# Kernel tuning notes

Hardware: AMD Instinct MI355X
Metric: run time of the kernel (lower is better)

The kernel has to match this reference:

```python
import jax, jax.numpy as jnp
import numpy as np

NN_SIZE = 10          # k for kNN (includes the point itself as its own nearest neighbor)
COS_EPS = 1e-8        # torch.nn.CosineSimilarity eps


def _pairwise_sqdist(p):
    # p: (B,N,3) -> (B,N,N) squared euclidean distances without (B,N,N,3) intermediate
    x2 = jnp.sum(p * p, axis=-1)                      # (B,N)
    inner = jnp.einsum('bnd,bmd->bnm', p, p)          # (B,N,N)
    return x2[:, :, None] + x2[:, None, :] - 2.0 * inner


def _batch_normals(points):
    # points: (B,N,3) -> PCA normals (B,N,3)
    d = _pairwise_sqdist(points)                      # (B,N,N)
    _, idx = jax.lax.top_k(-d, NN_SIZE)               # (B,N,K) indices of k nearest
    nbrs = jax.vmap(lambda p, i: p[i])(points, idx)   # (B,N,K,3) gathered neighborhoods
    centered = nbrs - jnp.mean(nbrs, axis=2, keepdims=True)
    cov = jnp.einsum('bnki,bnkj->bnij', centered, centered) / NN_SIZE  # (B,N,3,3)
    _, vecs = jnp.linalg.eigh(cov)                    # eigenvalues ascending
    return vecs[..., :, 0]                            # eigvec of smallest eigval = normal


def setup_inputs() -> dict:
    key = jax.random.key(0)
    k1, k2 = jax.random.split(key)
    pred = jax.random.normal(k1, (8, 4096, 3), dtype=jnp.float32)
    gt_normals = jax.random.normal(k2, (8, 4096, 3), dtype=jnp.float32)
    return {"pred": pred, "gt_normals": gt_normals}


def reference(pred, gt_normals):
    pred_normals = _batch_normals(pred)                         # (B,N,3)
    dot = jnp.sum(pred_normals * gt_normals, axis=-1)           # (B,N)
    na = jnp.linalg.norm(pred_normals, axis=-1)
    nb = jnp.linalg.norm(gt_normals, axis=-1)
    cos = dot / (jnp.maximum(na, COS_EPS) * jnp.maximum(nb, COS_EPS))
    return jnp.mean(1.0 - cos)
```

## Files before the change

### kernel.cpp

```cpp
#include <hip/hip_runtime.h>
#include <math.h>


#define NPTS   4096
#define KNN    10
#define NBINS  256
#define XLO    (-5.5f)
#define INVBW  (256.0f / 11.0f)
#define W      1536
#define QPB    32
#define NB     1024
#define LISTCAP 32768

__device__ __forceinline__ unsigned int umed3(unsigned int a, unsigned int b, unsigned int c) {
    unsigned int r;
    asm("v_med3_u32 %0, %1, %2, %3" : "=v"(r) : "v"(a), "v"(b), "v"(c));
    return r;
}

__device__ __forceinline__ void sift(unsigned int nd[KNN], unsigned int key) {
#pragma unroll
    for (int t = KNN - 1; t >= 1; --t)
        nd[t] = umed3(key, nd[t - 1], nd[t]);
    nd[0] = nd[0] < key ? nd[0] : key;
}

__device__ __forceinline__ int xbin(float x) {
    int bin = (int)floorf((x - XLO) * INVBW);
    return bin < 0 ? 0 : (bin > NBINS - 1 ? NBINS - 1 : bin);
}

#define MAKE_KEY(q, c, J)                                                     \
    ({                                                                        \
        float sw_ = (q).w + (c).w;                                            \
        float dp_ = fmaf((q).x, (c).x, fmaf((q).y, (c).y, (q).z * (c).z));    \
        float d_  = fmaf(-2.0f, dp_, sw_);                                    \
        d_ = fmaxf(d_, 0.0f);                                                 \
        (__float_as_uint(d_) & 0xFFFFF000u) | (unsigned)(J);                  \
    })

__device__ float normal_loss3f(const float nbx[KNN], const float nby[KNN],
                               const float nbz[KNN], const float* g3)
{
    float sx = 0.f, sy = 0.f, sz = 0.f;
#pragma unroll
    for (int t = 0; t < KNN; ++t) { sx += nbx[t]; sy += nby[t]; sz += nbz[t]; }
    float mx = sx * 0.1f, my = sy * 0.1f, mz = sz * 0.1f;
    float c00 = 0.f, c01 = 0.f, c02 = 0.f, c11 = 0.f, c12 = 0.f, c22 = 0.f;
#pragma unroll
    for (int t = 0; t < KNN; ++t) {
        float ux = nbx[t] - mx, uy = nby[t] - my, uz = nbz[t] - mz;
        c00 = fmaf(ux, ux, c00);
        c01 = fmaf(ux, uy, c01);
        c02 = fmaf(ux, uz, c02);
        c11 = fmaf(uy, uy, c11);
        c12 = fmaf(uy, uz, c12);
        c22 = fmaf(uz, uz, c22);
    }
    float a00 = c00 * 0.1f, a01 = c01 * 0.1f, a02 = c02 * 0.1f;
    float a11 = c11 * 0.1f, a12 = c12 * 0.1f, a22 = c22 * 0.1f;

    float vx = 1.0f, vy = 0.0f, vz = 0.0f;
    float qd = (a00 + a11 + a22) * (1.0f / 3.0f);
    float p1 = a01 * a01 + a02 * a02 + a12 * a12;
    float b00 = a00 - qd, b11 = a11 - qd, b22 = a22 - qd;
    float p2 = b00 * b00 + b11 * b11 + b22 * b22 + 2.0f * p1;
    if (p2 > 1e-30f) {
        float p   = sqrtf(p2 * (1.0f / 6.0f));
        float inv = 1.0f / p;
        float m00 = b00 * inv, m01 = a01 * inv, m02 = a02 * inv;
        float m11 = b11 * inv, m12 = a12 * inv, m22 = b22 * inv;
        float detB = m00 * (m11 * m22 - m12 * m12)
                   - m01 * (m01 * m22 - m12 * m02)
                   + m02 * (m01 * m12 - m11 * m02);
        float r = 0.5f * detB;
        r = r < -1.0f ? -1.0f : (r > 1.0f ? 1.0f : r);
        float phi  = acosf(r) * (1.0f / 3.0f);
        float eig0 = qd + 2.0f * p * cosf(phi + 2.0943951023931953f);
        float r0x = a00 - eig0, r0y = a01, r0z = a02;
        float r1y = a11 - eig0, r1z = a12;
        float r2z = a22 - eig0;
        float c0x = r0y * r1z - r0z * r1y;
        float c0y = r0z * r0y - r0x * r1z;
        float c0z = r0x * r1y - r0y * r0y;
        float c1x = r0y * r2z - r0z * r1z;
        float c1y = r0z * r0z - r0x * r2z;
        float c1z = r0x * r1z - r0y * r0z;
        float c2x = r1y * r2z - r1z * r1z;
        float c2y = r1z * r0z - r0y * r2z;
        float c2z = r0y * r1z - r1y * r0z;
        float n0 = c0x * c0x + c0y * c0y + c0z * c0z;
        float n1 = c1x * c1x + c1y * c1y + c1z * c1z;
        float n2 = c2x * c2x + c2y * c2y + c2z * c2z;
        float bx, by, bz, bn;
        if (n0 >= n1 && n0 >= n2) { bx = c0x; by = c0y; bz = c0z; bn = n0; }
        else if (n1 >= n2)        { bx = c1x; by = c1y; bz = c1z; bn = n1; }
        else                      { bx = c2x; by = c2y; bz = c2z; bn = n2; }
        if (bn > 1e-30f) {
            float s = rsqrtf(bn);
            vx = bx * s; vy = by * s; vz = bz * s;
        }
    }
    float gx = g3[0], gy = g3[1], gz = g3[2];
    float dotg = vx * gx + vy * gy + vz * gz;
    float na = sqrtf(vx * vx + vy * vy + vz * vz);
    float gn = sqrtf(gx * gx + gy * gy + gz * gz);
    float cs = dotg / (fmaxf(na, 1e-8f) * fmaxf(gn, 1e-8f));
    return 1.0f - cs;
}

__global__ __launch_bounds__(1024) void gtnl_bin(
    const float* __restrict__ pred, float4* __restrict__ wsPts,
    unsigned int* __restrict__ wsCnt)
{
    __shared__ unsigned int hist[NBINS];
    __shared__ unsigned int bst[NBINS + 1];

    const int tid = threadIdx.x;
    const int b   = blockIdx.x;
    if (b == 0 && tid == 0) wsCnt[0] = 0;
    const float* src = pred + (size_t)b * NPTS * 3;

    if (tid < NBINS) hist[tid] = 0;
    __syncthreads();

    float px[4], py[4], pz[4];
    int   pb[4], pidx[4];
#pragma unroll
    for (int k = 0; k < 4; ++k) {
        int p = tid + 1024 * k;
        float x = src[3 * p + 0];
        float y = src[3 * p + 1];
        float z = src[3 * p + 2];
        int bin = xbin(x);
        px[k] = x; py[k] = y; pz[k] = z; pb[k] = bin; pidx[k] = p;
        atomicAdd(&hist[bin], 1u);
    }
    __syncthreads();

    if (tid < 64) {
        unsigned s0 = hist[4 * tid + 0], s1 = hist[4 * tid + 1];
        unsigned s2 = hist[4 * tid + 2], s3 = hist[4 * tid + 3];
        unsigned tot = s0 + s1 + s2 + s3;
        unsigned pre = tot;
#pragma unroll
        for (int d = 1; d < 64; d <<= 1) {
            unsigned t = __shfl_up(pre, d, 64);
            if (tid >= d) pre += t;
        }
        unsigned ex = pre - tot;
        bst[4 * tid + 0] = ex;
        bst[4 * tid + 1] = ex + s0;
        bst[4 * tid + 2] = ex + s0 + s1;
        bst[4 * tid + 3] = ex + s0 + s1 + s2;
        if (tid == 63) bst[NBINS] = ex + tot;
    }
    __syncthreads();

    if (tid < NBINS) hist[tid] = bst[tid];
    __syncthreads();

#pragma unroll
    for (int k = 0; k < 4; ++k) {
        unsigned pos = atomicAdd(&hist[pb[k]], 1u);
        wsPts[(size_t)b * NPTS + pos] =
            make_float4(px[k], py[k], pz[k], __uint_as_float((unsigned)pidx[k]));
    }
}

__global__ __launch_bounds__(256, 8) void gtnl_scan(
    const float4* __restrict__ wsPts, const float* __restrict__ gt,
    float* __restrict__ qloss, unsigned int* __restrict__ wsCnt,
    unsigned int* __restrict__ wsList)
{
    __shared__ float4 pts[W];

    const int tid   = threadIdx.x;
    const int bid   = blockIdx.x;
    const int b     = bid >> 7;
    const int chunk = bid & 127;
    const int qbase = chunk * QPB;
    const int s     = tid & 7;
    const int ql    = tid >> 3;

    int W0 = qbase + QPB / 2 - W / 2;
    W0 = W0 < 0 ? 0 : (W0 > NPTS - W ? NPTS - W : W0);

    const float4* wp = wsPts + (size_t)b * NPTS;
    for (int i = tid; i < W; i += 256) {
        float4 v = wp[W0 + i];
        pts[i] = make_float4(v.x, v.y, v.z, fmaf(v.x, v.x, fmaf(v.y, v.y, v.z * v.z)));
    }
    __syncthreads();

    const int qpos = qbase + ql;
    const float4 q = pts[qpos - W0];

    unsigned int nd[KNN];
#pragma unroll
    for (int t = 0; t < KNN; ++t) nd[t] = 0x7F000000u;

#pragma unroll 2
    for (int t = 0; t < W / 8; ++t) {
        int j = 8 * t + s;
        float4 c = pts[j];
        sift(nd, MAKE_KEY(q, c, j));
    }

#pragma unroll
    for (int r = 1; r <= 4; r <<= 1) {
        unsigned int tmp[KNN];
#pragma unroll
        for (int t = 0; t < KNN; ++t) tmp[t] = nd[t];
#pragma unroll
        for (int t = 0; t < KNN; ++t) {
            unsigned int pk = (unsigned int)__shfl_xor((int)tmp[t], r, 64);
            sift(nd, pk);
        }
    }

    unsigned int thr_bits = (nd[KNN - 1] & 0xFFFFF000u) + 0x1000u;
    float thr = __uint_as_float(thr_bits);
    float hw  = __uint_as_float(__float_as_uint(sqrtf(thr)) + 4) + 1e-3f;
    bool okL = (W0 == 0)        || (q.x - hw > pts[0].x);
    bool okR = (W0 == NPTS - W) || (q.x + hw < pts[W - 1].x);

    const unsigned int qorig = __float_as_uint(wp[qpos].w);
    if (okL && okR) {
        float nbx[KNN], nby[KNN], nbz[KNN];
#pragma unroll
        for (int t = 0; t < KNN; ++t) {
            float4 pn = pts[nd[t] & 0xFFFu];
            nbx[t] = pn.x; nby[t] = pn.y; nbz[t] = pn.z;
        }
        float res = normal_loss3f(nbx, nby, nbz, gt + ((size_t)b * NPTS + qorig) * 3);
        if (s == 0) qloss[(size_t)b * NPTS + qorig] = res;
    } else {
        if (s == 0) {
            unsigned int idx = atomicAdd(wsCnt, 1u);
            wsList[idx] = ((unsigned)b << 12) | (unsigned)qpos;
            qloss[(size_t)b * NPTS + qorig] = 0.0f;
        }
    }
}

__global__ __launch_bounds__(256, 4) void gtnl_fix(
    const float4* __restrict__ wsPts, const float* __restrict__ gt,
    float* __restrict__ qloss, const unsigned int* __restrict__ wsCnt,
    const unsigned int* __restrict__ wsList)
{
    const int lane = threadIdx.x & 63;
    const int wid  = blockIdx.x * 4 + (threadIdx.x >> 6);
    unsigned int n = wsCnt[0];

    for (unsigned int i = wid; i < n; i += 4096) {
        unsigned int e = wsList[i];
        const int b    = e >> 12;
        const int qpos = e & 0xFFF;
        const float4* wp = wsPts + (size_t)b * NPTS;

        float4 qv = wp[qpos];
        float4 q  = make_float4(qv.x, qv.y, qv.z,
                                fmaf(qv.x, qv.x, fmaf(qv.y, qv.y, qv.z * qv.z)));
        const unsigned int qorig = __float_as_uint(qv.w);

        unsigned int nd[KNN];
#pragma unroll
        for (int t = 0; t < KNN; ++t) nd[t] = 0x7F000000u;

#pragma unroll 8
        for (int t = 0; t < NPTS / 64; ++t) {
            int j = 64 * t + lane;
            float4 v = wp[j];
            float4 c = make_float4(v.x, v.y, v.z,
                                   fmaf(v.x, v.x, fmaf(v.y, v.y, v.z * v.z)));
            sift(nd, MAKE_KEY(q, c, j));
        }

        unsigned int keys[KNN];
#pragma unroll
        for (int r = 0; r < KNN; ++r) {
            unsigned int m = nd[0];
#pragma unroll
            for (int d = 1; d < 64; d <<= 1) {
                unsigned int o = __shfl_xor(m, d, 64);
                m = m < o ? m : o;
            }
            keys[r] = m;
            bool win = (nd[0] == m);
#pragma unroll
            for (int t = 0; t < KNN - 1; ++t) nd[t] = win ? nd[t + 1] : nd[t];
            nd[KNN - 1] = win ? 0xFFFFFFFFu : nd[KNN - 1];
        }

        float nbx[KNN], nby[KNN], nbz[KNN];
#pragma unroll
        for (int t = 0; t < KNN; ++t) {
            float4 pn = wp[keys[t] & 0xFFFu];
            nbx[t] = pn.x; nby[t] = pn.y; nbz[t] = pn.z;
        }
        float res = normal_loss3f(nbx, nby, nbz, gt + ((size_t)b * NPTS + qorig) * 3);
        if (lane == 0) qloss[(size_t)b * NPTS + qorig] = res;
    }
}

__global__ __launch_bounds__(1024) void gtnl_reduceQ(
    const float* __restrict__ qloss, float* __restrict__ out)
{
    __shared__ float sbuf[1024];
    const int tid = threadIdx.x;
    const float4* q4 = (const float4*)qloss;
    float s = 0.0f;
#pragma unroll
    for (int t = 0; t < 8; ++t) {
        float4 v = q4[tid + 1024 * t];
        s += (v.x + v.y) + (v.z + v.w);
    }
    sbuf[tid] = s;
    __syncthreads();
    for (int k = 512; k > 0; k >>= 1) {
        if (tid < k) sbuf[tid] += sbuf[tid + k];
        __syncthreads();
    }
    if (tid == 0) out[0] = sbuf[0] / 32768.0f;
}

__global__ __launch_bounds__(256) void gtnl_brute(
    const float* __restrict__ pred, const float* __restrict__ gt,
    float* __restrict__ partial)
{
    __shared__ float4 ptsB[NPTS];
    __shared__ unsigned int mbuf[64][3][KNN];

    const int tid = threadIdx.x;
    const int b   = blockIdx.x >> 6;
    const int qc  = blockIdx.x & 63;
    const int ql  = tid & 63;
    const int sub = tid >> 6;
    const int qi  = qc * 64 + ql;

    const float* src = pred + (size_t)b * NPTS * 3;
    for (int p = tid; p < NPTS; p += 256) {
        float x = src[3 * p + 0], y = src[3 * p + 1], z = src[3 * p + 2];
        ptsB[p] = make_float4(x, y, z, fmaf(x, x, fmaf(y, y, z * z)));
    }
    __syncthreads();

    const float4 q = ptsB[qi];
    unsigned int nd[KNN];
#pragma unroll
    for (int t = 0; t < KNN; ++t) nd[t] = 0xFFFFFFFFu;

    const int j0 = sub * 1024;
#pragma unroll 8
    for (int j = j0; j < j0 + 1024; ++j) {
        float4 c = ptsB[j];
        sift(nd, MAKE_KEY(q, c, j));
    }

    if (sub != 0) {
#pragma unroll
        for (int t = 0; t < KNN; ++t) mbuf[ql][sub - 1][t] = nd[t];
    }
    __syncthreads();

    float res = 0.0f;
    if (sub == 0) {
#pragma unroll
        for (int ss = 0; ss < 3; ++ss)
#pragma unroll
            for (int t = 0; t < KNN; ++t) sift(nd, mbuf[ql][ss][t]);
        float nbx[KNN], nby[KNN], nbz[KNN];
#pragma unroll
        for (int t = 0; t < KNN; ++t) {
            float4 pn = ptsB[nd[t] & 0xFFFu];
            nbx[t] = pn.x; nby[t] = pn.y; nbz[t] = pn.z;
        }
        res = normal_loss3f(nbx, nby, nbz, gt + ((size_t)b * NPTS + qi) * 3);
#pragma unroll
        for (int d = 32; d > 0; d >>= 1) res += __shfl_xor(res, d, 64);
    }
    __syncthreads();
    if (tid == 0) partial[blockIdx.x] = res;
}

__global__ __launch_bounds__(512) void gtnl_reduceP(
    const float* __restrict__ partial, float* __restrict__ out)
{
    __shared__ float sb[512];
    const int tid = threadIdx.x;
    sb[tid] = partial[tid];
    __syncthreads();
    for (int k = 256; k > 0; k >>= 1) {
        if (tid < k) sb[tid] += sb[tid + k];
        __syncthreads();
    }
    if (tid == 0) out[0] = sb[0] / 32768.0f;
}

extern "C" void kernel_launch(void* const* d_in, const int* in_sizes, int n_in,
                              void* d_out, int out_size, void* d_ws, size_t ws_size,
                              hipStream_t stream) {
    const float* pred = (const float*)d_in[0];
    const float* gt   = (const float*)d_in[1];
    float* out        = (float*)d_out;

    const size_t PTS_BYTES   = (size_t)8 * NPTS * sizeof(float4);
    const size_t QLOSS_BYTES = (size_t)8 * NPTS * sizeof(float);
    const size_t LIST_BYTES  = (size_t)LISTCAP * sizeof(unsigned);
    const size_t NEED = PTS_BYTES + QLOSS_BYTES + LIST_BYTES + 64;

    if (ws_size >= NEED) {
        float4*       wsPts  = (float4*)d_ws;
        float*        qloss  = (float*)((char*)d_ws + PTS_BYTES);
        unsigned int* wsList = (unsigned int*)((char*)d_ws + PTS_BYTES + QLOSS_BYTES);
        unsigned int* wsCnt  = (unsigned int*)((char*)d_ws + PTS_BYTES + QLOSS_BYTES + LIST_BYTES);

        gtnl_bin<<<8, 1024, 0, stream>>>(pred, wsPts, wsCnt);
        gtnl_scan<<<NB, 256, 0, stream>>>(wsPts, gt, qloss, wsCnt, wsList);
        gtnl_fix<<<NB, 256, 0, stream>>>(wsPts, gt, qloss, wsCnt, wsList);
        gtnl_reduceQ<<<1, 1024, 0, stream>>>(qloss, out);
    } else {
        float* partial = (float*)d_ws;
        gtnl_brute<<<512, 256, 0, stream>>>(pred, gt, partial);
        gtnl_reduceP<<<1, 512, 0, stream>>>(partial, out);
    }
}
```

Before: 54.19 us.

## Scan kNN window outward from center with early termination on x-distance bound

Reorders the shared-memory window so candidates are stored in alternating order outward from the query chunk center, enlarges the window, and adds a wave-wide early exit once both sides exceed the current kth-neighbor distance in x. Candidate insertions are also skipped when no lane would improve its top-k list. This aims to cut the number of distance evaluations and sifts per query and reduce fallback cases, at the cost of larger shared memory (lower occupancy via launch bounds 4) and extra divergence and ballot checks.

```diff
diff --git a/kernel.cpp b/kernel.cpp
--- a/kernel.cpp
+++ b/kernel.cpp
@@ -7,7 +7,7 @@
 #define NBINS  256
 #define XLO    (-5.5f)
 #define INVBW  (256.0f / 11.0f)
-#define W      1536
+#define W      2048
 #define QPB    32
 #define NB     1024
 #define LISTCAP 32768
@@ -168,7 +168,7 @@
     }
 }
 
-__global__ __launch_bounds__(256, 8) void gtnl_scan(
+__global__ __launch_bounds__(256, 4) void gtnl_scan(
     const float4* __restrict__ wsPts, const float* __restrict__ gt,
     float* __restrict__ qloss, unsigned int* __restrict__ wsCnt,
     unsigned int* __restrict__ wsList)
@@ -187,24 +187,49 @@
     W0 = W0 < 0 ? 0 : (W0 > NPTS - W ? NPTS - W : W0);
 
     const float4* wp = wsPts + (size_t)b * NPTS;
+
+    const int c0 = qbase + QPB / 2 - W0;
+    const int mL = c0, mR = W - c0;
+    const int m2 = 2 * (mL < mR ? mL : mR);
     for (int i = tid; i < W; i += 256) {
-        float4 v = wp[W0 + i];
+        int j;
+        if (i < m2) j = (i & 1) ? (c0 - 1 - (i >> 1)) : (c0 + (i >> 1));
+        else        j = (mL <= mR) ? i : (W - 1 - i);
+        float4 v = wp[W0 + j];
         pts[i] = make_float4(v.x, v.y, v.z, fmaf(v.x, v.x, fmaf(v.y, v.y, v.z * v.z)));
     }
     __syncthreads();
 
     const int qpos = qbase + ql;
-    const float4 q = pts[qpos - W0];
+    const int off  = qpos - W0;
+    const int qslot = (off >= c0) ? 2 * (off - c0) : 2 * (c0 - 1 - off) + 1;
+    const float4 q = pts[qslot];
 
     unsigned int nd[KNN];
 #pragma unroll
     for (int t = 0; t < KNN; ++t) nd[t] = 0x7F000000u;
 
-#pragma unroll 2
-    for (int t = 0; t < W / 8; ++t) {
-        int j = 8 * t + s;
-        float4 c = pts[j];
-        sift(nd, MAKE_KEY(q, c, j));
+    bool dR = false, dL = false;
+    for (int tt = 0; tt < W / 32; ++tt) {
+        const int base = 32 * tt + s;
+        float lsdx = 0.0f;
+        unsigned int ldxk = 0;
+#pragma unroll
+        for (int u = 0; u < 4; ++u) {
+            int j = base + 8 * u;
+            float4 c = pts[j];
+            float sdx = c.x - q.x;
+            float dp = fmaf(q.x, c.x, fmaf(q.y, c.y, q.z * c.z));
+            float d  = fmaf(-2.0f, dp, q.w + c.w);
+            d = fmaxf(d, 0.0f);
+            unsigned int key = (__float_as_uint(d) & 0xFFFFF000u) | (unsigned)j;
+            if (__any(key < nd[KNN - 1])) sift(nd, key);
+            if (u == 3) { lsdx = sdx; ldxk = __float_as_uint(sdx * sdx) & 0xFFFFF000u; }
+        }
+        bool far = ldxk > nd[KNN - 1];
+        dR = dR || (far && lsdx >= 0.0f);
+        dL = dL || (far && lsdx <= 0.0f);
+        if (__all(dR && dL)) break;
     }
 
 #pragma unroll
@@ -222,8 +247,10 @@
     unsigned int thr_bits = (nd[KNN - 1] & 0xFFFFF000u) + 0x1000u;
     float thr = __uint_as_float(thr_bits);
     float hw  = __uint_as_float(__float_as_uint(sqrtf(thr)) + 4) + 1e-3f;
-    bool okL = (W0 == 0)        || (q.x - hw > pts[0].x);
-    bool okR = (W0 == NPTS - W) || (q.x + hw < pts[W - 1].x);
+    float xlo = wp[W0].x;
+    float xhi = wp[W0 + W - 1].x;
+    bool okL = (W0 == 0)        || (q.x - hw > xlo);
+    bool okR = (W0 == NPTS - W) || (q.x + hw < xhi);
 
     const unsigned int qorig = __float_as_uint(wp[qpos].w);
     if (okL && okR) {
```

Result: slower. 64.86 us (+19.7%).

## Bound fallback kNN scan by x-bin range and halve queries per block

Applied to the files above, without the earlier changes.

The scan kernel now handles 16 queries per block with 16 lanes per query. That doubles the block count and shortens each lane's serial sift loop, at the cost of one extra shuffle-merge round. The bin kernel saves its per-batch bin prefix offsets, and the scan kernel records each failed query's search half-width. The fix kernel uses both to scan only the x-sorted slice that can hold true neighbours, instead of all 4096 points. This adds workspace buffers and a masked tail, and depends on the stored threshold being conservative.

```diff
diff --git a/kernel.cpp b/kernel.cpp
--- a/kernel.cpp
+++ b/kernel.cpp
@@ -8,8 +8,8 @@
 #define XLO    (-5.5f)
 #define INVBW  (256.0f / 11.0f)
 #define W      1536
-#define QPB    32
-#define NB     1024
+#define QPB    16
+#define NB     2048
 #define LISTCAP 32768
 
 __device__ __forceinline__ unsigned int umed3(unsigned int a, unsigned int b, unsigned int c) {
@@ -111,7 +111,7 @@
 
 __global__ __launch_bounds__(1024) void gtnl_bin(
     const float* __restrict__ pred, float4* __restrict__ wsPts,
-    unsigned int* __restrict__ wsCnt)
+    unsigned int* __restrict__ wsBins, unsigned int* __restrict__ wsCnt)
 {
     __shared__ unsigned int hist[NBINS];
     __shared__ unsigned int bst[NBINS + 1];
@@ -166,22 +166,24 @@
         wsPts[(size_t)b * NPTS + pos] =
             make_float4(px[k], py[k], pz[k], __uint_as_float((unsigned)pidx[k]));
     }
-}
-
-__global__ __launch_bounds__(256, 8) void gtnl_scan(
+    if (tid < NBINS) wsBins[b * (NBINS + 1) + tid] = bst[tid];
+    if (tid == 0)    wsBins[b * (NBINS + 1) + NBINS] = bst[NBINS];
+}
+
+__global__ __launch_bounds__(256, 6) void gtnl_scan(
     const float4* __restrict__ wsPts, const float* __restrict__ gt,
     float* __restrict__ qloss, unsigned int* __restrict__ wsCnt,
-    unsigned int* __restrict__ wsList)
+    unsigned int* __restrict__ wsList, float* __restrict__ wsThr)
 {
     __shared__ float4 pts[W];
 
     const int tid   = threadIdx.x;
     const int bid   = blockIdx.x;
-    const int b     = bid >> 7;
-    const int chunk = bid & 127;
+    const int b     = bid >> 8;
+    const int chunk = bid & 255;
     const int qbase = chunk * QPB;
-    const int s     = tid & 7;
-    const int ql    = tid >> 3;
+    const int s     = tid & 15;
+    const int ql    = tid >> 4;
 
     int W0 = qbase + QPB / 2 - W / 2;
     W0 = W0 < 0 ? 0 : (W0 > NPTS - W ? NPTS - W : W0);
@@ -200,15 +202,15 @@
 #pragma unroll
     for (int t = 0; t < KNN; ++t) nd[t] = 0x7F000000u;
 
-#pragma unroll 2
-    for (int t = 0; t < W / 8; ++t) {
-        int j = 8 * t + s;
+#pragma unroll 8
+    for (int t = 0; t < W / 16; ++t) {
+        int j = 16 * t + s;
         float4 c = pts[j];
         sift(nd, MAKE_KEY(q, c, j));
     }
 
 #pragma unroll
-    for (int r = 1; r <= 4; r <<= 1) {
+    for (int r = 1; r <= 8; r <<= 1) {
         unsigned int tmp[KNN];
 #pragma unroll
         for (int t = 0; t < KNN; ++t) tmp[t] = nd[t];
@@ -239,15 +241,17 @@
         if (s == 0) {
             unsigned int idx = atomicAdd(wsCnt, 1u);
             wsList[idx] = ((unsigned)b << 12) | (unsigned)qpos;
+            wsThr[idx]  = hw;
             qloss[(size_t)b * NPTS + qorig] = 0.0f;
         }
     }
 }
 
 __global__ __launch_bounds__(256, 4) void gtnl_fix(
-    const float4* __restrict__ wsPts, const float* __restrict__ gt,
-    float* __restrict__ qloss, const unsigned int* __restrict__ wsCnt,
-    const unsigned int* __restrict__ wsList)
+    const float4* __restrict__ wsPts, const unsigned int* __restrict__ wsBins,
+    const float* __restrict__ gt, float* __restrict__ qloss,
+    const unsigned int* __restrict__ wsCnt, const unsigned int* __restrict__ wsList,
+    const float* __restrict__ wsThr)
 {
     const int lane = threadIdx.x & 63;
     const int wid  = blockIdx.x * 4 + (threadIdx.x >> 6);
@@ -257,24 +261,31 @@
         unsigned int e = wsList[i];
         const int b    = e >> 12;
         const int qpos = e & 0xFFF;
+        const float hw = wsThr[i];
         const float4* wp = wsPts + (size_t)b * NPTS;
+        const unsigned int* bst = wsBins + b * (NBINS + 1);
 
         float4 qv = wp[qpos];
         float4 q  = make_float4(qv.x, qv.y, qv.z,
                                 fmaf(qv.x, qv.x, fmaf(qv.y, qv.y, qv.z * qv.z)));
         const unsigned int qorig = __float_as_uint(qv.w);
 
+        const int jlo = (int)bst[xbin(qv.x - hw)];
+        const int jhi = (int)bst[xbin(qv.x + hw) + 1];
+
         unsigned int nd[KNN];
 #pragma unroll
         for (int t = 0; t < KNN; ++t) nd[t] = 0x7F000000u;
 
-#pragma unroll 8
-        for (int t = 0; t < NPTS / 64; ++t) {
-            int j = 64 * t + lane;
-            float4 v = wp[j];
+        for (int j0 = jlo; j0 < jhi; j0 += 64) {
+            int j = j0 + lane;
+            int js = j < jhi ? j : jhi - 1;
+            float4 v = wp[js];
             float4 c = make_float4(v.x, v.y, v.z,
                                    fmaf(v.x, v.x, fmaf(v.y, v.y, v.z * v.z)));
-            sift(nd, MAKE_KEY(q, c, j));
+            unsigned int key = MAKE_KEY(q, c, js);
+            key = j < jhi ? key : 0xFFFFFFFFu;
+            sift(nd, key);
         }
 
         unsigned int keys[KNN];
@@ -408,17 +419,22 @@
     const size_t PTS_BYTES   = (size_t)8 * NPTS * sizeof(float4);
     const size_t QLOSS_BYTES = (size_t)8 * NPTS * sizeof(float);
     const size_t LIST_BYTES  = (size_t)LISTCAP * sizeof(unsigned);
-    const size_t NEED = PTS_BYTES + QLOSS_BYTES + LIST_BYTES + 64;
+    const size_t THR_BYTES   = (size_t)LISTCAP * sizeof(float);
+    const size_t BINS_BYTES  = (size_t)8 * (NBINS + 1) * sizeof(unsigned);
+    const size_t NEED = PTS_BYTES + QLOSS_BYTES + LIST_BYTES + THR_BYTES + BINS_BYTES + 64;
 
     if (ws_size >= NEED) {
-        float4*       wsPts  = (float4*)d_ws;
-        float*        qloss  = (float*)((char*)d_ws + PTS_BYTES);
-        unsigned int* wsList = (unsigned int*)((char*)d_ws + PTS_BYTES + QLOSS_BYTES);
-        unsigned int* wsCnt  = (unsigned int*)((char*)d_ws + PTS_BYTES + QLOSS_BYTES + LIST_BYTES);
-
-        gtnl_bin<<<8, 1024, 0, stream>>>(pred, wsPts, wsCnt);
-        gtnl_scan<<<NB, 256, 0, stream>>>(wsPts, gt, qloss, wsCnt, wsList);
-        gtnl_fix<<<NB, 256, 0, stream>>>(wsPts, gt, qloss, wsCnt, wsList);
+        char* p = (char*)d_ws;
+        float4*       wsPts  = (float4*)p;                 p += PTS_BYTES;
+        float*        qloss  = (float*)p;                  p += QLOSS_BYTES;
+        unsigned int* wsList = (unsigned int*)p;           p += LIST_BYTES;
+        float*        wsThr  = (float*)p;                  p += THR_BYTES;
+        unsigned int* wsBins = (unsigned int*)p;           p += BINS_BYTES;
+        unsigned int* wsCnt  = (unsigned int*)p;
+
+        gtnl_bin<<<8, 1024, 0, stream>>>(pred, wsPts, wsBins, wsCnt);
+        gtnl_scan<<<NB, 256, 0, stream>>>(wsPts, gt, qloss, wsCnt, wsList, wsThr);
+        gtnl_fix<<<1024, 256, 0, stream>>>(wsPts, wsBins, gt, qloss, wsCnt, wsList, wsThr);
         gtnl_reduceQ<<<1, 1024, 0, stream>>>(qloss, out);
     } else {
         float* partial = (float*)d_ws;
```

New measurement: 61.28 us. 13.1% more time.
